# Kernel tuning notes

Hardware: AMD Instinct MI355X
Metric: run time of the kernel (lower is better)

## Reference

```python
import jax, jax.numpy as jnp
import numpy as np

OUT_H, OUT_W = 736, 240  # hardcoded interpolate target in the module


def resize_bilinear_ac(x, out_h, out_w):
    # bilinear, align_corners=True, NCHW
    B, C, H, W = x.shape
    def lin(n_in, n_out):
        pos = jnp.arange(n_out, dtype=jnp.float32) * (float(n_in - 1) / float(n_out - 1))
        i0 = jnp.floor(pos).astype(jnp.int32)
        i1 = jnp.minimum(i0 + 1, n_in - 1)
        f = pos - i0.astype(jnp.float32)
        return i0, i1, f
    hi0, hi1, hf = lin(H, out_h)
    xh = (x[:, :, hi0, :] * (1.0 - hf)[None, None, :, None]
          + x[:, :, hi1, :] * hf[None, None, :, None])
    wi0, wi1, wf = lin(W, out_w)
    return xh[..., wi0] * (1.0 - wf) + xh[..., wi1] * wf


def setup_inputs() -> dict:
    key = jax.random.key(0)
    x = jax.random.normal(key, (32, 7, 368, 120), dtype=jnp.float32)
    w = np.ones((6, 1, 1, 2), dtype=np.float32)
    w[:, :, :, 1] = -1.0  # fixed [1, -1] horizontal edge filter, depthwise
    return {"x": x, "dw_weight": jnp.asarray(w)}


def reference(x, dw_weight):
    C = x.shape[1]
    xi = resize_bilinear_ac(x, OUT_H, OUT_W)              # [B,C,736,240]
    lab = jnp.argmax(xi, axis=1)                          # [B,736,240]
    lab = jnp.transpose(lab, (0, 2, 1))                   # [B,240,736]
    oh = jax.nn.one_hot(lab, C, axis=1, dtype=jnp.float32)  # [B,C,240,736]

    # --- out1: depthwise [1,-1] diff with right pad of 0.5, relu, flipped argmax ---
    d = oh[:, :C - 1]                                     # drop background channel
    padded = jnp.pad(d, ((0, 0), (0, 0), (0, 0), (0, 1)), constant_values=0.5)
    w0 = dw_weight[:, 0, 0, 0][None, :, None, None]
    w1 = dw_weight[:, 0, 0, 1][None, :, None, None]
    edge = jax.nn.relu(padded[..., :-1] * w0 + padded[..., 1:] * w1)  # [B,C-1,240,736]
    t = jnp.transpose(edge, (0, 3, 2, 1))                 # [B,736,240,C-1]
    t = jnp.flip(t, axis=1)
    out1 = jnp.argmax(t, axis=1, keepdims=True)           # [B,1,240,C-1] int

    # --- out2: background channel summed over 8 bands of 30 rows ---
    xr = oh[:, -1]                                        # [B,240,736]
    B = xr.shape[0]
    out2 = xr.reshape(B, 8, 30, OUT_H).sum(axis=(2, 3)).reshape(B, 1, 8)
    return out1, out2
```

## Files before the change

kernel.cpp:

```cpp
#include <hip/hip_runtime.h>
#include <hip/hip_bf16.h>
#include <float.h>

#define BB 32
#define CC 7
#define IH 368
#define IW 120
#define OH 736
#define OW 240
#define NCH 23
#define CHROWS 32

#define OUT1_ELEMS (BB * OW * 6)

#define LAB_BYTES (BB * OH * OW)

__global__ __launch_bounds__(256) void labels_kernel(
    const float* __restrict__ x, unsigned char* __restrict__ lab) {
  int idx = blockIdx.x * blockDim.x + threadIdx.x;
  if (idx >= BB * OH * OW) return;

  int w = idx % OW;
  int t = idx / OW;
  int h = t % OH;
  int b = t / OH;

  const float RH = (float)(367.0 / 735.0);
  const float RW = (float)(119.0 / 239.0);

  float ph = __fmul_rn((float)h, RH);
  int hi0 = (int)floorf(ph);
  int hi1 = min(hi0 + 1, IH - 1);
  float hf = __fsub_rn(ph, (float)hi0);

  float pw = __fmul_rn((float)w, RW);
  int wi0 = (int)floorf(pw);
  int wi1 = min(wi0 + 1, IW - 1);
  float wf = __fsub_rn(pw, (float)wi0);

  float omhf = __fsub_rn(1.0f, hf);
  float omwf = __fsub_rn(1.0f, wf);

  const float* xb = x + (size_t)b * CC * IH * IW;
  int o00 = hi0 * IW + wi0;
  int o01 = hi0 * IW + wi1;
  int o10 = hi1 * IW + wi0;
  int o11 = hi1 * IW + wi1;

  float best = -FLT_MAX;
  int bc = 0;
#pragma unroll
  for (int c = 0; c < CC; ++c) {
    const float* xc = xb + c * (IH * IW);
    float x00 = xc[o00];
    float x01 = xc[o01];
    float x10 = xc[o10];
    float x11 = xc[o11];
    float a = __fadd_rn(__fmul_rn(x00, omhf), __fmul_rn(x10, hf));
    float bcol = __fadd_rn(__fmul_rn(x01, omhf), __fmul_rn(x11, hf));
    float v = __fadd_rn(__fmul_rn(a, omwf), __fmul_rn(bcol, wf));
    if (v > best) { best = v; bc = c; }
  }
  lab[idx] = (unsigned char)bc;
}

__global__ __launch_bounds__(256) void edge_partial_kernel(
    const unsigned char* __restrict__ lab, unsigned long long* __restrict__ part) {
  int blk = blockIdx.x;
  int b = blk / NCH;
  int k = blk % NCH;
  int w = threadIdx.x;
  if (w >= OW) return;

  int h0 = k * CHROWS;
  int nrows = (h0 + CHROWS + 1 <= OH) ? (CHROWS + 1) : (OH - h0);

  const unsigned char* L = lab + (size_t)b * OH * OW + (size_t)h0 * OW + w;

  unsigned e0 = 0, e1 = 0, e2 = 0, e3 = 0, e4 = 0, e5 = 0;
  int prev = L[0];
  int c6 = (prev == 6);
#pragma unroll 8
  for (int hl = 1; hl < nrows; ++hl) {
    int cur = L[(size_t)hl * OW];
    if (hl <= CHROWS - 1) c6 += (cur == 6);
    if (cur != prev) {
      e0 = (prev == 0) ? (unsigned)hl : e0;
      e1 = (prev == 1) ? (unsigned)hl : e1;
      e2 = (prev == 2) ? (unsigned)hl : e2;
      e3 = (prev == 3) ? (unsigned)hl : e3;
      e4 = (prev == 4) ? (unsigned)hl : e4;
      e5 = (prev == 5) ? (unsigned)hl : e5;
    }
    prev = cur;
  }

  unsigned long long u =
      (unsigned long long)e0 | ((unsigned long long)e1 << 8) |
      ((unsigned long long)e2 << 16) | ((unsigned long long)e3 << 24) |
      ((unsigned long long)e4 << 32) | ((unsigned long long)e5 << 40) |
      ((unsigned long long)(unsigned)c6 << 48);
  part[(size_t)(b * NCH + k) * OW + w] = u;
}

__global__ __launch_bounds__(256) void finalize_kernel(
    const unsigned long long* __restrict__ part, float* __restrict__ out) {
  int b = blockIdx.x;
  int w = threadIdx.x;

  __shared__ int cnt[256];

  int c6 = 0;
  if (w < OW) {
    int g0 = -1, g1 = -1, g2 = -1, g3 = -1, g4 = -1, g5 = -1;
    const unsigned long long* P = part + (size_t)b * NCH * OW + w;
#pragma unroll
    for (int k = 0; k < NCH; ++k) {
      unsigned long long u = P[(size_t)k * OW];
      int base = k * CHROWS - 1;
      unsigned v;
      v = (unsigned)(u) & 0xffu;        if (v) g0 = base + (int)v;
      v = (unsigned)(u >> 8) & 0xffu;   if (v) g1 = base + (int)v;
      v = (unsigned)(u >> 16) & 0xffu;  if (v) g2 = base + (int)v;
      v = (unsigned)(u >> 24) & 0xffu;  if (v) g3 = base + (int)v;
      v = (unsigned)(u >> 32) & 0xffu;  if (v) g4 = base + (int)v;
      v = (unsigned)(u >> 40) & 0xffu;  if (v) g5 = base + (int)v;
      c6 += (int)((u >> 48) & 0xffu);
    }
    float* o1 = out + (size_t)b * (OW * 6) + w * 6;
    o1[0] = (g0 >= 0) ? (float)(735 - g0) : 0.0f;
    o1[1] = (g1 >= 0) ? (float)(735 - g1) : 0.0f;
    o1[2] = (g2 >= 0) ? (float)(735 - g2) : 0.0f;
    o1[3] = (g3 >= 0) ? (float)(735 - g3) : 0.0f;
    o1[4] = (g4 >= 0) ? (float)(735 - g4) : 0.0f;
    o1[5] = (g5 >= 0) ? (float)(735 - g5) : 0.0f;
  }

  cnt[threadIdx.x] = (w < OW) ? c6 : 0;
  __syncthreads();
  if (threadIdx.x < 8) {
    int s = 0;
#pragma unroll
    for (int i = 0; i < 30; ++i) s += cnt[threadIdx.x * 30 + i];
    out[OUT1_ELEMS + b * 8 + threadIdx.x] = (float)s;
  }
}

extern "C" void kernel_launch(void* const* d_in, const int* in_sizes, int n_in,
                              void* d_out, int out_size, void* d_ws, size_t ws_size,
                              hipStream_t stream) {
  const float* x = (const float*)d_in[0];
  float* out = (float*)d_out;
  unsigned char* lab = (unsigned char*)d_ws;
  unsigned long long* part =
      (unsigned long long*)((char*)d_ws + LAB_BYTES);

  int total = BB * OH * OW;
  int blocks1 = (total + 255) / 256;
  labels_kernel<<<blocks1, 256, 0, stream>>>(x, lab);
  edge_partial_kernel<<<BB * NCH, 256, 0, stream>>>(lab, part);
  finalize_kernel<<<BB, 256, 0, stream>>>(part, out);
}
```

Baseline: 113.6 us.

## Fuse label computation into edge scan with sliding-row register reuse

Merges the bilinear-resize argmax label kernel into the per-column edge scan, so the byte label map no longer goes to global memory and is not read back. Each thread walks its rows and keeps the two source rows for all channels in registers, reloading only when the source row index advances. Chunk height is halved to 16 rows so that 46 chunks per batch keep enough blocks in flight, at the cost of more partial records and more recomputed overlap rows. The row-by-row loop is serial per thread, so fewer threads now wait on dependent loads.

```diff
diff --git a/kernel.cpp b/kernel.cpp
--- a/kernel.cpp
+++ b/kernel.cpp
@@ -8,83 +8,83 @@
 #define IW 120
 #define OH 736
 #define OW 240
-#define NCH 23
-#define CHROWS 32
+#define NCH 46
+#define CHROWS 16
 
 #define OUT1_ELEMS (BB * OW * 6)
 
-#define LAB_BYTES (BB * OH * OW)
-
-__global__ __launch_bounds__(256) void labels_kernel(
-    const float* __restrict__ x, unsigned char* __restrict__ lab) {
-  int idx = blockIdx.x * blockDim.x + threadIdx.x;
-  if (idx >= BB * OH * OW) return;
-
-  int w = idx % OW;
-  int t = idx / OW;
-  int h = t % OH;
-  int b = t / OH;
-
-  const float RH = (float)(367.0 / 735.0);
-  const float RW = (float)(119.0 / 239.0);
-
-  float ph = __fmul_rn((float)h, RH);
-  int hi0 = (int)floorf(ph);
-  int hi1 = min(hi0 + 1, IH - 1);
-  float hf = __fsub_rn(ph, (float)hi0);
-
-  float pw = __fmul_rn((float)w, RW);
-  int wi0 = (int)floorf(pw);
-  int wi1 = min(wi0 + 1, IW - 1);
-  float wf = __fsub_rn(pw, (float)wi0);
-
-  float omhf = __fsub_rn(1.0f, hf);
-  float omwf = __fsub_rn(1.0f, wf);
-
-  const float* xb = x + (size_t)b * CC * IH * IW;
-  int o00 = hi0 * IW + wi0;
-  int o01 = hi0 * IW + wi1;
-  int o10 = hi1 * IW + wi0;
-  int o11 = hi1 * IW + wi1;
-
-  float best = -FLT_MAX;
-  int bc = 0;
-#pragma unroll
-  for (int c = 0; c < CC; ++c) {
-    const float* xc = xb + c * (IH * IW);
-    float x00 = xc[o00];
-    float x01 = xc[o01];
-    float x10 = xc[o10];
-    float x11 = xc[o11];
-    float a = __fadd_rn(__fmul_rn(x00, omhf), __fmul_rn(x10, hf));
-    float bcol = __fadd_rn(__fmul_rn(x01, omhf), __fmul_rn(x11, hf));
-    float v = __fadd_rn(__fmul_rn(a, omwf), __fmul_rn(bcol, wf));
-    if (v > best) { best = v; bc = c; }
-  }
-  lab[idx] = (unsigned char)bc;
-}
-
-__global__ __launch_bounds__(256) void edge_partial_kernel(
-    const unsigned char* __restrict__ lab, unsigned long long* __restrict__ part) {
+__global__ __launch_bounds__(256) void fused_label_edge_kernel(
+    const float* __restrict__ x, unsigned long long* __restrict__ part) {
   int blk = blockIdx.x;
   int b = blk / NCH;
   int k = blk % NCH;
   int w = threadIdx.x;
   if (w >= OW) return;
 
+  const float RH = (float)(367.0 / 735.0);
+  const float RW = (float)(119.0 / 239.0);
+
+  float pw = __fmul_rn((float)w, RW);
+  int wi0 = (int)floorf(pw);
+  int wi1 = min(wi0 + 1, IW - 1);
+  float wf = __fsub_rn(pw, (float)wi0);
+  float omwf = __fsub_rn(1.0f, wf);
+
   int h0 = k * CHROWS;
-  int nrows = (h0 + CHROWS + 1 <= OH) ? (CHROWS + 1) : (OH - h0);
+  int nrows = min(CHROWS + 1, OH - h0);
 
-  const unsigned char* L = lab + (size_t)b * OH * OW + (size_t)h0 * OW + w;
+  const float* xb = x + (size_t)b * CC * IH * IW;
+
+  float t00[CC], t01[CC], t10[CC], t11[CC];
+  int cur = -2;
 
   unsigned e0 = 0, e1 = 0, e2 = 0, e3 = 0, e4 = 0, e5 = 0;
-  int prev = L[0];
-  int c6 = (prev == 6);
-#pragma unroll 8
-  for (int hl = 1; hl < nrows; ++hl) {
-    int cur = L[(size_t)hl * OW];
-    if (hl <= CHROWS - 1) c6 += (cur == 6);
-    if (cur != prev) {
+  int c6 = 0;
+  int prev = -1;
+
+  for (int hl = 0; hl < nrows; ++hl) {
+    int h = h0 + hl;
+    float ph = __fmul_rn((float)h, RH);
+    int hi0 = (int)floorf(ph);
+    float hf = __fsub_rn(ph, (float)hi0);
+    float omhf = __fsub_rn(1.0f, hf);
+    int hi1 = min(hi0 + 1, IH - 1);
+
+    if (hi0 == cur + 1) {
+#pragma unroll
+      for (int c = 0; c < CC; ++c) {
+        t00[c] = t10[c];
+        t01[c] = t11[c];
+        const float* rp = xb + c * (IH * IW) + hi1 * IW;
+        t10[c] = rp[wi0];
+        t11[c] = rp[wi1];
+      }
+      cur = hi0;
+    } else if (hi0 != cur) {
+#pragma unroll
+      for (int c = 0; c < CC; ++c) {
+        const float* r0 = xb + c * (IH * IW) + hi0 * IW;
+        const float* r1 = xb + c * (IH * IW) + hi1 * IW;
+        t00[c] = r0[wi0];
+        t01[c] = r0[wi1];
+        t10[c] = r1[wi0];
+        t11[c] = r1[wi1];
+      }
+      cur = hi0;
+    }
+
+    float best = -FLT_MAX;
+    int bc = 0;
+#pragma unroll
+    for (int c = 0; c < CC; ++c) {
+      float va = __fadd_rn(__fmul_rn(t00[c], omhf), __fmul_rn(t10[c], hf));
+      float vb = __fadd_rn(__fmul_rn(t01[c], omhf), __fmul_rn(t11[c], hf));
+      float v = __fadd_rn(__fmul_rn(va, omwf), __fmul_rn(vb, wf));
+      if (v > best) { best = v; bc = c; }
+    }
+
+    if (hl < CHROWS) c6 += (bc == 6);
+    if (hl > 0 && bc != prev) {
       e0 = (prev == 0) ? (unsigned)hl : e0;
       e1 = (prev == 1) ? (unsigned)hl : e1;
       e2 = (prev == 2) ? (unsigned)hl : e2;
@@ -92,7 +92,7 @@
       e4 = (prev == 4) ? (unsigned)hl : e4;
       e5 = (prev == 5) ? (unsigned)hl : e5;
     }
-    prev = cur;
+    prev = bc;
   }
 
   unsigned long long u =
@@ -151,13 +151,8 @@
                               hipStream_t stream) {
   const float* x = (const float*)d_in[0];
   float* out = (float*)d_out;
-  unsigned char* lab = (unsigned char*)d_ws;
-  unsigned long long* part =
-      (unsigned long long*)((char*)d_ws + LAB_BYTES);
+  unsigned long long* part = (unsigned long long*)d_ws;
 
-  int total = BB * OH * OW;
-  int blocks1 = (total + 255) / 256;
-  labels_kernel<<<blocks1, 256, 0, stream>>>(x, lab);
-  edge_partial_kernel<<<BB * NCH, 256, 0, stream>>>(lab, part);
+  fused_label_edge_kernel<<<BB * NCH, 256, 0, stream>>>(x, part);
   finalize_kernel<<<BB, 256, 0, stream>>>(part, out);
 }
```

Measured after the change: 100.1 us. 1.13x faster.
